# Optimization experiments

Hardware: AMD Instinct MI355X
Metric: run time of the kernel (lower is better)

## Reference

```python
import jax, jax.numpy as jnp
import numpy as np

H, KV, D, HID = 32, 8, 128, 4096
B, S = 1, 2048
ROPE_THETA = 10000.0


def setup_inputs() -> dict:
    key = jax.random.key(0)
    ks = jax.random.split(key, 5)
    std = 0.02
    return {
        "x": jax.random.normal(ks[0], (B, S, HID), jnp.float32),
        "Wq": jax.random.normal(ks[1], (H * D, HID), jnp.float32) * std,
        "Wk": jax.random.normal(ks[2], (KV * D, HID), jnp.float32) * std,
        "Wv": jax.random.normal(ks[3], (KV * D, HID), jnp.float32) * std,
        "Wo": jax.random.normal(ks[4], (HID, H * D), jnp.float32) * std,
    }


def _rope_cos_sin(seq_len, dim, dtype):
    inv_freq = 1.0 / (ROPE_THETA ** (jnp.arange(0, dim, 2, dtype=jnp.float32) / dim))
    t = jnp.arange(seq_len, dtype=jnp.float32)
    freqs = jnp.einsum("s,d->sd", t, inv_freq)          # [S, D/2]
    emb = jnp.concatenate([freqs, freqs], axis=-1)        # [S, D]
    return jnp.cos(emb).astype(dtype), jnp.sin(emb).astype(dtype)


def _rotate_half(x):
    x1, x2 = jnp.split(x, 2, axis=-1)
    return jnp.concatenate([-x2, x1], axis=-1)


def reference(x, Wq, Wk, Wv, Wo):
    Bx, Sx, _ = x.shape
    q = (x @ Wq.T).reshape(Bx, Sx, H, D).transpose(0, 2, 1, 3)    # [B,H,S,D]
    k = (x @ Wk.T).reshape(Bx, Sx, KV, D).transpose(0, 2, 1, 3)   # [B,KV,S,D]
    v = (x @ Wv.T).reshape(Bx, Sx, KV, D).transpose(0, 2, 1, 3)

    cos, sin = _rope_cos_sin(Sx, D, x.dtype)                       # [S,D]
    q = q * cos + _rotate_half(q) * sin
    k = k * cos + _rotate_half(k) * sin

    rep = H // KV
    k = jnp.repeat(k, rep, axis=1)                                 # [B,H,S,D]
    v = jnp.repeat(v, rep, axis=1)

    scale = 1.0 / jnp.sqrt(jnp.asarray(D, x.dtype))
    scores = jnp.einsum("bhqd,bhkd->bhqk", q, k) * scale           # [B,H,S,S]
    causal = jnp.tril(jnp.ones((Sx, Sx), dtype=bool))
    scores = jnp.where(causal, scores, jnp.asarray(-1e30, x.dtype))
    attn = jax.nn.softmax(scores, axis=-1)
    out = jnp.einsum("bhqk,bhkd->bhqd", attn, v)                   # [B,H,S,D]
    out = out.transpose(0, 2, 1, 3).reshape(Bx, Sx, H * D)
    return out @ Wo.T
```

## Files before the change

### kernel.cpp

```cpp
#include <hip/hip_runtime.h>

typedef unsigned short u16;
typedef unsigned int u32;

using f32x4  = __attribute__((ext_vector_type(4))) float;
using f32x16 = __attribute__((ext_vector_type(16))) float;
using bf16x8 = __attribute__((ext_vector_type(8))) __bf16;

#define S_LEN 2048
#define HID_DIM 4096
#define NH 32
#define NKV 8
#define HD 128
#define QKVN 6144

__device__ __forceinline__ u16 f2b(float f) {
  union { float f; u32 u; } v; v.f = f;
  u32 r = (v.u + 0x7FFFu + ((v.u >> 16) & 1u)) >> 16;
  return (u16)r;
}
__device__ __forceinline__ float b2f(u16 b) {
  union { u32 u; float f; } v; v.u = ((u32)b) << 16;
  return v.f;
}

__device__ __forceinline__ u32 cvtpk_bf16(float lo, float hi) {
  u32 r;
  asm("v_cvt_pk_bf16_f32 %0, %1, %2" : "=v"(r) : "v"(lo), "v"(hi));
  return r;
}
__device__ __forceinline__ void plane_swap(u32& a, u32& b) {
  asm volatile("v_permlane32_swap_b32 %0, %1" : "+v"(a), "+v"(b));
}

#define AS1 __attribute__((address_space(1)))
#define AS3 __attribute__((address_space(3)))
__device__ __forceinline__ void gl_lds16(const u16* g, u16* l) {
  __builtin_amdgcn_global_load_lds((const AS1 u32*)g, (AS3 u32*)l, 16, 0, 0);
}

#define SBAR  __builtin_amdgcn_s_barrier()
#define SCHED0 __builtin_amdgcn_sched_barrier(0)
#define LGKM0 do { asm volatile("s_waitcnt lgkmcnt(0)" ::: "memory"); SCHED0; } while (0)
#define PRIO1 __builtin_amdgcn_s_setprio(1)
#define PRIO0 __builtin_amdgcn_s_setprio(0)

template <int N> __device__ __forceinline__ void waitv() {
  if constexpr (N == 0)      asm volatile("s_waitcnt vmcnt(0)" ::: "memory");
  else if constexpr (N == 6) asm volatile("s_waitcnt vmcnt(6)" ::: "memory");
  else if constexpr (N == 7) asm volatile("s_waitcnt vmcnt(7)" ::: "memory");
  else                       asm volatile("s_waitcnt vmcnt(0)" ::: "memory");
  SCHED0;
}

__global__ void cast_kernel(const float* __restrict__ src, u16* __restrict__ dst, int n4) {
  int i = blockIdx.x * blockDim.x + threadIdx.x;
  int stride = gridDim.x * blockDim.x;
  for (; i < n4; i += stride) {
    float4 v = ((const float4*)src)[i];
    uint2 o;
    o.x = (u32)f2b(v.x) | ((u32)f2b(v.y) << 16);
    o.y = (u32)f2b(v.z) | ((u32)f2b(v.w) << 16);
    ((uint2*)dst)[i] = o;
  }
}


#define STAGE(DST, SRC, CH, LDK)                                   \
  _Pragma("unroll") for (int c = 0; c < (CH); ++c) {               \
    int d_ = c * 8192 + tid * 16;                                  \
    int rw_ = d_ >> 7;                                             \
    int cb_ = (d_ & 127) ^ ((rw_ & 7) << 4);                       \
    gl_lds16((SRC) + (size_t)rw_ * (LDK) + (cb_ >> 1), (DST) + (d_ >> 1)); \
  }

#define RDA(ABUF, MLO, KS)                                                    \
  _Pragma("unroll") for (int mm = 0; mm < 4; ++mm)                            \
    af[(MLO) + mm][KS] = *(const bf16x8*)((const char*)(ABUF) +               \
      (wmo + ((MLO) + mm) * 16 + lr) * 128 + (((((KS) << 2) | lg) ^ lr7) << 4));

#define RDB(BBUF, KS)                                                         \
  _Pragma("unroll") for (int nn = 0; nn < NF; ++nn)                           \
    bfr[nn][KS] = *(const bf16x8*)((const char*)(BBUF) +                      \
      (wno + nn * 16 + lr) * 128 + (((((KS) << 2) | lg) ^ lr7) << 4));

#define MFMA_Q(MLO, KS)                                                       \
  _Pragma("unroll") for (int mm = 0; mm < 4; ++mm)                            \
  _Pragma("unroll") for (int nn = 0; nn < NF; ++nn)                           \
    acc[(MLO) + mm][nn] = __builtin_amdgcn_mfma_f32_16x16x32_bf16(            \
        af[(MLO) + mm][KS], bfr[nn][KS], acc[(MLO) + mm][nn], 0, 0, 0);

template <int BN, int WN, int CBF>
__global__ __launch_bounds__(512, 2) void gemm8p(
    const u16* __restrict__ A, const u16* __restrict__ B, void* __restrict__ Cout,
    int M, int N, int K)
{
  constexpr int BM = 256;
  constexpr int NF = WN / 16;
  constexpr int LA = BM / 64;
  constexpr int LB = BN / 64;
  constexpr int LT = LA + LB;
  extern __shared__ __align__(16) u16 smem[];
  u16* const As0 = smem;
  u16* const Bs0 = smem + 2 * BM * 64;

  const int tid  = threadIdx.x;
  const int lane = tid & 63;
  const int wave = tid >> 6;
  const int lr  = lane & 15;
  const int lg  = lane >> 4;
  const int lr7 = lane & 7;

  const int nbx = N / BN;
  const int bid = blockIdx.x;
  const int cpx = gridDim.x >> 3;
  const int swz = (bid & 7) * cpx + (bid >> 3);
  const int bm = (swz / nbx) * BM;
  const int bn = (swz % nbx) * BN;
  const int wmo = (wave >> 2) * 128;
  const int wno = (wave & 3) * WN;

  const int NT = K >> 6;

  f32x4 acc[8][NF] = {};
  bf16x8 af[8][2], bfr[NF][2];

  const u16* aP = A + (size_t)bm * K;
  const u16* bP = B + (size_t)bn * K;

  STAGE(As0,           aP,      LA, K);
  STAGE(Bs0,           bP,      LB, K);
  STAGE(As0 + BM * 64, aP + 64, LA, K);
  STAGE(Bs0 + BN * 64, bP + 64, LB, K);
  waitv<LT>();
  SBAR; SCHED0;

  for (int t = 0; t < NT; ++t) {
    const int buf = t & 1;
    const u16* ab = As0 + buf * (BM * 64);
    const u16* bb = Bs0 + buf * (BN * 64);
    const bool st = (t + 2 < NT);

    RDA(ab, 0, 0); RDA(ab, 4, 0); RDB(bb, 0);
    LGKM0;
    PRIO1; MFMA_Q(0, 0); MFMA_Q(4, 0); PRIO0;
    RDA(ab, 0, 1); RDA(ab, 4, 1); RDB(bb, 1);
    LGKM0;
    SBAR;

    if (st) {
      STAGE(As0 + buf * (BM * 64), aP + (size_t)(t + 2) * 64, LA, K);
      STAGE(Bs0 + buf * (BN * 64), bP + (size_t)(t + 2) * 64, LB, K);
    }
    PRIO1; MFMA_Q(0, 1); MFMA_Q(4, 1); PRIO0;
    if (t + 1 < NT) {
      if (st) waitv<LT>(); else waitv<0>();
    }
    SBAR; SCHED0;
  }

#pragma unroll
  for (int m = 0; m < 8; ++m)
#pragma unroll
    for (int j = 0; j < 4; ++j) {
      int row = bm + wmo + m * 16 + lg * 4 + j;
      size_t base = (size_t)row * N + bn + wno + lr;
      if constexpr (CBF) {
        u16* C = (u16*)Cout;
#pragma unroll
        for (int nn = 0; nn < NF; ++nn) C[base + nn * 16] = f2b(acc[m][nn][j]);
      } else {
        float* C = (float*)Cout;
#pragma unroll
        for (int nn = 0; nn < NF; ++nn) C[base + nn * 16] = acc[m][nn][j];
      }
    }
}

__global__ void rope_qk(const u16* __restrict__ qkv, u16* __restrict__ dst,
                        int col_off, float scale, int frag) {
  int idx = blockIdx.x * blockDim.x + threadIdx.x;
  int i = idx & 63;
  int s = (idx >> 6) & (S_LEN - 1);
  int h = idx >> 17;
  const u16* row = qkv + (size_t)s * QKVN + col_off + h * HD;
  float a = b2f(row[i]);
  float b = b2f(row[i + 64]);
  float invf = __expf(-(float)i * 0.14391156831212787f);
  float f = (float)s * invf;
  float sn, cs;
  sincosf(f, &sn, &cs);
  float o1 = (a * cs - b * sn) * scale;
  float o2 = (b * cs + a * sn) * scale;
  if (frag) {
    int qt = h * 64 + (s >> 5);
    int qq = s & 31;
    int i2 = i + 64;
    dst[((qt * 8 + (i  >> 4)) * 2 + ((i  >> 3) & 1)) * 256 + qq * 8 + (i  & 7)] = f2b(o1);
    dst[((qt * 8 + (i2 >> 4)) * 2 + ((i2 >> 3) & 1)) * 256 + qq * 8 + (i2 & 7)] = f2b(o2);
  } else {
    u16* orow = dst + ((size_t)h * S_LEN + s) * HD;
    orow[i]      = f2b(o1);
    orow[i + 64] = f2b(o2);
  }
}

__global__ __launch_bounds__(256) void vf_pack(const u16* __restrict__ qkv,
                                               u16* __restrict__ VF) {
  __shared__ u16 vlds[32][136];
  const int bid = blockIdx.x;
  const int kv = bid >> 6, t = bid & 63;
  const int tid = threadIdx.x;
  const int r = tid >> 3, d0 = (tid & 7) * 16;
  const u16* src = qkv + (size_t)(t * 32 + r) * QKVN + 5120 + kv * HD + d0;
  *(bf16x8*)&vlds[r][d0]     = *(const bf16x8*)src;
  *(bf16x8*)&vlds[r][d0 + 8] = *(const bf16x8*)(src + 8);
  __syncthreads();
  u16* outt = VF + (size_t)bid * 4096;
#pragma unroll
  for (int g = 0; g < 2; ++g) {
    int G = tid + g * 256;
    int q = G & 31, dt = (G >> 5) & 3, hi2 = (G >> 7) & 1, kc = G >> 8;
    union { u16 u[8]; uint4 v; } o;
#pragma unroll
    for (int e = 0; e < 8; ++e)
      o.u[e] = vlds[kc * 16 + hi2 * 8 + e][dt * 32 + q];
    *(uint4*)&outt[G * 8] = o.v;
  }
}

__global__ __launch_bounds__(256, 2) void attn_fwd(
    const u16* __restrict__ QF,
    const u16* __restrict__ KF,
    const u16* __restrict__ VF,
    u16* __restrict__ Out)
{
  const int tid  = threadIdx.x;
  const int lane = tid & 63;
  const int wv   = tid >> 6;
  const int q31  = lane & 31;
  const int hi   = lane >> 5;
  const int bid  = blockIdx.x;
  const int kvh  = bid & 7;
  const int qi   = 63 - (bid >> 3);
  const int q0   = qi * 32;
  const int h    = kvh * 4 + wv;
  const int nt   = qi + 1;

  const u16* kbase = KF + (size_t)kvh * 64 * 4096 + hi * 256  + q31 * 8;
  const u16* vbase = VF + (size_t)kvh * 64 * 4096 + hi * 1024 + q31 * 8;

  bf16x8 qf[8];
  const u16* qfp = QF + (size_t)(h * 64 + qi) * 4096 + hi * 256 + q31 * 8;
#pragma unroll
  for (int dc = 0; dc < 8; ++dc)
    qf[dc] = *(const bf16x8*)(qfp + dc * 512);

  f32x16 o0 = {}, o1 = {}, o2 = {}, o3 = {};
  float m = -1e30f, lsum = 0.f;

  for (int t = 0; t < nt; ++t) {
    SBAR;

    bf16x8 kf[8];
    const u16* kfp = kbase + (size_t)t * 4096;
#pragma unroll
    for (int dc = 0; dc < 8; ++dc)
      kf[dc] = *(const bf16x8*)(kfp + dc * 512);

    bf16x8 vf[8];
    const u16* vfp = vbase + (size_t)t * 4096;
#pragma unroll
    for (int i = 0; i < 8; ++i)
      vf[i] = *(const bf16x8*)(vfp + (i & 1) * 2048 + (i >> 1) * 256);

    f32x16 st = {};
    PRIO1;
#pragma unroll
    for (int dc = 0; dc < 8; ++dc)
      st = __builtin_amdgcn_mfma_f32_32x32x16_bf16(kf[dc], qf[dc], st, 0, 0, 0);
    PRIO0;

    if (t == nt - 1) {
#pragma unroll
      for (int r = 0; r < 16; ++r) {
        int kk = (r & 3) + 8 * (r >> 2) + 4 * hi;
        if (kk > q31) st[r] = -1e30f;
      }
    }

    float a0 = fmaxf(st[0], st[1]),   a1 = fmaxf(st[2], st[3]);
    float a2 = fmaxf(st[4], st[5]),   a3 = fmaxf(st[6], st[7]);
    float a4 = fmaxf(st[8], st[9]),   a5 = fmaxf(st[10], st[11]);
    float a6 = fmaxf(st[12], st[13]), a7 = fmaxf(st[14], st[15]);
    a0 = fmaxf(a0, a1); a2 = fmaxf(a2, a3); a4 = fmaxf(a4, a5); a6 = fmaxf(a6, a7);
    float pmax = fmaxf(fmaxf(a0, a2), fmaxf(a4, a6));
    pmax = fmaxf(pmax, __shfl_xor(pmax, 32));

    if (__any(pmax > m + 8.f)) {
      float mn = fmaxf(m, pmax);
      float sf = exp2f(m - mn);
      m = mn;
      lsum *= sf;
#pragma unroll
      for (int r = 0; r < 16; ++r) { o0[r] *= sf; o1[r] *= sf; o2[r] *= sf; o3[r] *= sf; }
    }

    float ev[16];
#pragma unroll
    for (int r = 0; r < 16; ++r) ev[r] = exp2f(st[r] - m);
    float s0 = (ev[0] + ev[1]) + (ev[2] + ev[3]);
    float s1 = (ev[4] + ev[5]) + (ev[6] + ev[7]);
    float s2 = (ev[8] + ev[9]) + (ev[10] + ev[11]);
    float s3 = (ev[12] + ev[13]) + (ev[14] + ev[15]);
    float ps = (s0 + s1) + (s2 + s3);
    ps += __shfl_xor(ps, 32);
    lsum += ps;

    u32 c0 = cvtpk_bf16(ev[0],  ev[1]),  c1 = cvtpk_bf16(ev[2],  ev[3]);
    u32 c2 = cvtpk_bf16(ev[4],  ev[5]),  c3 = cvtpk_bf16(ev[6],  ev[7]);
    u32 c4 = cvtpk_bf16(ev[8],  ev[9]),  c5 = cvtpk_bf16(ev[10], ev[11]);
    u32 c6 = cvtpk_bf16(ev[12], ev[13]), c7 = cvtpk_bf16(ev[14], ev[15]);
    plane_swap(c0, c2);
    plane_swap(c1, c3);
    plane_swap(c4, c6);
    plane_swap(c5, c7);
    union { u32 u[4]; bf16x8 v; } pb0u, pb1u;
    pb0u.u[0] = c0; pb0u.u[1] = c1; pb0u.u[2] = c2; pb0u.u[3] = c3;
    pb1u.u[0] = c4; pb1u.u[1] = c5; pb1u.u[2] = c6; pb1u.u[3] = c7;

    PRIO1;
    o0 = __builtin_amdgcn_mfma_f32_32x32x16_bf16(vf[0], pb0u.v, o0, 0, 0, 0);
    o1 = __builtin_amdgcn_mfma_f32_32x32x16_bf16(vf[2], pb0u.v, o1, 0, 0, 0);
    o2 = __builtin_amdgcn_mfma_f32_32x32x16_bf16(vf[4], pb0u.v, o2, 0, 0, 0);
    o3 = __builtin_amdgcn_mfma_f32_32x32x16_bf16(vf[6], pb0u.v, o3, 0, 0, 0);
    o0 = __builtin_amdgcn_mfma_f32_32x32x16_bf16(vf[1], pb1u.v, o0, 0, 0, 0);
    o1 = __builtin_amdgcn_mfma_f32_32x32x16_bf16(vf[3], pb1u.v, o1, 0, 0, 0);
    o2 = __builtin_amdgcn_mfma_f32_32x32x16_bf16(vf[5], pb1u.v, o2, 0, 0, 0);
    o3 = __builtin_amdgcn_mfma_f32_32x32x16_bf16(vf[7], pb1u.v, o3, 0, 0, 0);
    PRIO0;
  }

  float inv = 1.0f / lsum;
  u16* orow = Out + (size_t)(q0 + q31) * (NH * HD) + h * HD;
#pragma unroll
  for (int dt = 0; dt < 4; ++dt) {
    const f32x16& oo = dt == 0 ? o0 : dt == 1 ? o1 : dt == 2 ? o2 : o3;
#pragma unroll
    for (int g = 0; g < 4; ++g) {
      ushort4 pk;
      pk.x = f2b(oo[g * 4 + 0] * inv);
      pk.y = f2b(oo[g * 4 + 1] * inv);
      pk.z = f2b(oo[g * 4 + 2] * inv);
      pk.w = f2b(oo[g * 4 + 3] * inv);
      *(ushort4*)&orow[dt * 32 + 8 * g + 4 * hi] = pk;
    }
  }
}

extern "C" void kernel_launch(void* const* d_in, const int* in_sizes, int n_in,
                              void* d_out, int out_size, void* d_ws, size_t ws_size,
                              hipStream_t stream) {
  const float* x  = (const float*)d_in[0];
  const float* Wq = (const float*)d_in[1];
  const float* Wk = (const float*)d_in[2];
  const float* Wv = (const float*)d_in[3];
  const float* Wo = (const float*)d_in[4];
  float* out = (float*)d_out;

  char* ws = (char*)d_ws;
  u16* xb   = (u16*)(ws);
  u16* wqkv = (u16*)(ws + (16ull << 20));
  u16* wo_b = (u16*)(ws + (64ull << 20));
  u16* qkvb = (u16*)(ws + (96ull << 20));
  u16* qb   = (u16*)(ws + (16ull << 20));
  u16* kfb  = (u16*)(ws + (32ull << 20));
  u16* vfb  = (u16*)(ws + (36ull << 20));
  u16* ao   = (u16*)(ws);

  const int smem_q = (256 + 192) * 256;
  const int smem_o = (256 + 128) * 256;
  hipFuncSetAttribute((const void*)&gemm8p<192, 48, 1>,
                      hipFuncAttributeMaxDynamicSharedMemorySize, smem_q);
  hipFuncSetAttribute((const void*)&gemm8p<128, 32, 0>,
                      hipFuncAttributeMaxDynamicSharedMemorySize, smem_o);

  cast_kernel<<<4096, 256, 0, stream>>>(x,  xb,   (2048 * 4096) / 4);
  cast_kernel<<<4096, 256, 0, stream>>>(Wq, wqkv, (4096 * 4096) / 4);
  cast_kernel<<<2048, 256, 0, stream>>>(Wk, wqkv + (size_t)4096 * 4096, (1024 * 4096) / 4);
  cast_kernel<<<2048, 256, 0, stream>>>(Wv, wqkv + (size_t)5120 * 4096, (1024 * 4096) / 4);
  cast_kernel<<<4096, 256, 0, stream>>>(Wo, wo_b, (4096 * 4096) / 4);

  gemm8p<192, 48, 1><<<256, 512, smem_q, stream>>>(xb, wqkv, qkvb, 2048, 6144, 4096);

  rope_qk<<<(32 * 2048 * 64) / 256, 256, 0, stream>>>(qkvb, qb,  0,    0.12751741f, 1);
  rope_qk<<<(8  * 2048 * 64) / 256, 256, 0, stream>>>(qkvb, kfb, 4096, 1.0f,        1);
  vf_pack<<<512, 256, 0, stream>>>(qkvb, vfb);

  attn_fwd<<<512, 256, 0, stream>>>(qb, kfb, vfb, ao);

  gemm8p<128, 32, 0><<<256, 512, smem_o, stream>>>(ao, wo_b, out, 2048, 4096, 4096);
}
```

Baseline: 312.9 us.

## Add finer-grained pipelined QKV GEMM and retile output projection GEMM

Adds a new QKV projection GEMM kernel that splits each K-step into four M-quarter MFMA phases. Global-to-LDS staging of the next tile is interleaved across those phases with a shallower vmcnt wait, to overlap loads with compute more finely and cut the live A-fragment registers. The output projection GEMM is generalized over BM and switched to a 128x256 tile with 64-wide wave columns, which changes reuse and the register footprint. The extra barriers per step add sync overhead and risk stalls.

```diff
diff --git a/kernel.cpp b/kernel.cpp
--- a/kernel.cpp
+++ b/kernel.cpp
@@ -47,6 +47,7 @@
 
 template <int N> __device__ __forceinline__ void waitv() {
   if constexpr (N == 0)      asm volatile("s_waitcnt vmcnt(0)" ::: "memory");
+  else if constexpr (N == 3) asm volatile("s_waitcnt vmcnt(3)" ::: "memory");
   else if constexpr (N == 6) asm volatile("s_waitcnt vmcnt(6)" ::: "memory");
   else if constexpr (N == 7) asm volatile("s_waitcnt vmcnt(7)" ::: "memory");
   else                       asm volatile("s_waitcnt vmcnt(0)" ::: "memory");
@@ -65,7 +66,6 @@
   }
 }
 
-
 #define STAGE(DST, SRC, CH, LDK)                                   \
   _Pragma("unroll") for (int c = 0; c < (CH); ++c) {               \
     int d_ = c * 8192 + tid * 16;                                  \
@@ -74,6 +74,109 @@
     gl_lds16((SRC) + (size_t)rw_ * (LDK) + (cb_ >> 1), (DST) + (d_ >> 1)); \
   }
 
+#define RAF(S, MQ)                                                            \
+  _Pragma("unroll") for (int j = 0; j < 2; ++j)                               \
+  _Pragma("unroll") for (int ks = 0; ks < 2; ++ks)                            \
+    af[j][ks] = *(const bf16x8*)((const char*)(As + (S)*16384) +              \
+      (wmo + (MQ)*32 + j*16 + lr) * 128 + ((((ks << 2) | lg) ^ lr7) << 4));
+
+#define RBF(S)                                                                \
+  _Pragma("unroll") for (int nn = 0; nn < 3; ++nn)                            \
+  _Pragma("unroll") for (int ks = 0; ks < 2; ++ks)                            \
+    bfr[nn][ks] = *(const bf16x8*)((const char*)(Bs + (S)*12288) +            \
+      (wno + nn*16 + lr) * 128 + ((((ks << 2) | lg) ^ lr7) << 4));
+
+#define MQUAD(MQ)                                                             \
+  _Pragma("unroll") for (int ks = 0; ks < 2; ++ks)                            \
+  _Pragma("unroll") for (int j = 0; j < 2; ++j)                               \
+  _Pragma("unroll") for (int nn = 0; nn < 3; ++nn)                            \
+    acc[(MQ)*2 + j][nn] = __builtin_amdgcn_mfma_f32_16x16x32_bf16(            \
+        af[j][ks], bfr[nn][ks], acc[(MQ)*2 + j][nn], 0, 0, 0);
+
+#define SGA(T, H) if ((T) < NT) { STAGE(As + ((T)&1)*16384 + (H)*8192,        \
+      aP + (size_t)((H)*128) * K + (size_t)(T)*64, 2, K); }
+#define SGB(T)    if ((T) < NT) { STAGE(Bs + ((T)&1)*12288,                   \
+      bP + (size_t)(T)*64, 3, K); }
+
+__global__ __launch_bounds__(512, 2) void gemm8s(
+    const u16* __restrict__ A, const u16* __restrict__ B, u16* __restrict__ C,
+    int M, int N, int K)
+{
+  extern __shared__ __align__(16) u16 smem[];
+  u16* const As = smem;
+  u16* const Bs = smem + 32768;
+
+  const int tid  = threadIdx.x;
+  const int lane = tid & 63;
+  const int wave = tid >> 6;
+  const int lr  = lane & 15;
+  const int lg  = lane >> 4;
+  const int lr7 = lane & 7;
+
+  const int nbx = N / 192;
+  const int bid = blockIdx.x;
+  const int cpx = gridDim.x >> 3;
+  const int swz = (bid & 7) * cpx + (bid >> 3);
+  const int bm = (swz / nbx) * 256;
+  const int bn = (swz % nbx) * 192;
+  const int wmo = (wave >> 2) * 128;
+  const int wno = (wave & 3) * 48;
+
+  const int NT = K >> 6;
+
+  f32x4 acc[8][3] = {};
+  bf16x8 af[2][2], bfr[3][2];
+
+  const u16* aP = A + (size_t)bm * K;
+  const u16* bP = B + (size_t)bn * K;
+
+  SGA(0, 0); SGA(0, 1); SGB(0); SGB(1);
+  waitv<3>();
+  SBAR; SCHED0;
+
+  for (int E = 0; E < NT; E += 2) {
+    const int O = E + 1;
+    RAF(0, 0); RBF(0); SGA(O, 0);
+    SCHED0; SBAR; LGKM0;
+    PRIO1; MQUAD(0); PRIO0; SBAR; SCHED0;
+    RAF(0, 1); SGA(O, 1); SGB(E + 2);
+    SCHED0; SBAR; LGKM0;
+    PRIO1; MQUAD(1); PRIO0; SBAR; SCHED0;
+    RAF(0, 2);
+    SCHED0; SBAR; LGKM0;
+    PRIO1; MQUAD(2); PRIO0; SBAR; SCHED0;
+    RAF(0, 3);
+    SCHED0; SBAR; LGKM0;
+    PRIO1; MQUAD(3); PRIO0;
+    if (E + 2 < NT) waitv<3>(); else waitv<0>();
+    SBAR; SCHED0;
+    RAF(1, 0); RBF(1); SGA(E + 2, 0);
+    SCHED0; SBAR; LGKM0;
+    PRIO1; MQUAD(0); PRIO0; SBAR; SCHED0;
+    RAF(1, 1); SGA(E + 2, 1); SGB(O + 2);
+    SCHED0; SBAR; LGKM0;
+    PRIO1; MQUAD(1); PRIO0; SBAR; SCHED0;
+    RAF(1, 2);
+    SCHED0; SBAR; LGKM0;
+    PRIO1; MQUAD(2); PRIO0; SBAR; SCHED0;
+    RAF(1, 3);
+    SCHED0; SBAR; LGKM0;
+    PRIO1; MQUAD(3); PRIO0;
+    if (O + 2 < NT) waitv<3>(); else waitv<0>();
+    SBAR; SCHED0;
+  }
+
+#pragma unroll
+  for (int m = 0; m < 8; ++m)
+#pragma unroll
+    for (int j = 0; j < 4; ++j) {
+      int row = bm + wmo + m * 16 + lg * 4 + j;
+      size_t base = (size_t)row * N + bn + wno + lr;
+#pragma unroll
+      for (int nn = 0; nn < 3; ++nn) C[base + nn * 16] = f2b(acc[m][nn][j]);
+    }
+}
+
 #define RDA(ABUF, MLO, KS)                                                    \
   _Pragma("unroll") for (int mm = 0; mm < 4; ++mm)                            \
     af[(MLO) + mm][KS] = *(const bf16x8*)((const char*)(ABUF) +               \
@@ -90,12 +193,12 @@
     acc[(MLO) + mm][nn] = __builtin_amdgcn_mfma_f32_16x16x32_bf16(            \
         af[(MLO) + mm][KS], bfr[nn][KS], acc[(MLO) + mm][nn], 0, 0, 0);
 
-template <int BN, int WN, int CBF>
+template <int BM, int BN, int WN, int CBF>
 __global__ __launch_bounds__(512, 2) void gemm8p(
     const u16* __restrict__ A, const u16* __restrict__ B, void* __restrict__ Cout,
     int M, int N, int K)
 {
-  constexpr int BM = 256;
+  constexpr int MF = BM / 32;
   constexpr int NF = WN / 16;
   constexpr int LA = BM / 64;
   constexpr int LB = BN / 64;
@@ -117,13 +220,13 @@
   const int swz = (bid & 7) * cpx + (bid >> 3);
   const int bm = (swz / nbx) * BM;
   const int bn = (swz % nbx) * BN;
-  const int wmo = (wave >> 2) * 128;
+  const int wmo = (wave >> 2) * (BM / 2);
   const int wno = (wave & 3) * WN;
 
   const int NT = K >> 6;
 
-  f32x4 acc[8][NF] = {};
-  bf16x8 af[8][2], bfr[NF][2];
+  f32x4 acc[MF][NF] = {};
+  bf16x8 af[MF][2], bfr[NF][2];
 
   const u16* aP = A + (size_t)bm * K;
   const u16* bP = B + (size_t)bn * K;
@@ -141,10 +244,14 @@
     const u16* bb = Bs0 + buf * (BN * 64);
     const bool st = (t + 2 < NT);
 
-    RDA(ab, 0, 0); RDA(ab, 4, 0); RDB(bb, 0);
+    RDA(ab, 0, 0);
+    if constexpr (MF == 8) { RDA(ab, 4, 0); }
+    RDB(bb, 0);
     LGKM0;
-    PRIO1; MFMA_Q(0, 0); MFMA_Q(4, 0); PRIO0;
-    RDA(ab, 0, 1); RDA(ab, 4, 1); RDB(bb, 1);
+    PRIO1; MFMA_Q(0, 0); if constexpr (MF == 8) { MFMA_Q(4, 0); } PRIO0;
+    RDA(ab, 0, 1);
+    if constexpr (MF == 8) { RDA(ab, 4, 1); }
+    RDB(bb, 1);
     LGKM0;
     SBAR;
 
@@ -152,7 +259,7 @@
       STAGE(As0 + buf * (BM * 64), aP + (size_t)(t + 2) * 64, LA, K);
       STAGE(Bs0 + buf * (BN * 64), bP + (size_t)(t + 2) * 64, LB, K);
     }
-    PRIO1; MFMA_Q(0, 1); MFMA_Q(4, 1); PRIO0;
+    PRIO1; MFMA_Q(0, 1); if constexpr (MF == 8) { MFMA_Q(4, 1); } PRIO0;
     if (t + 1 < NT) {
       if (st) waitv<LT>(); else waitv<0>();
     }
@@ -160,7 +267,7 @@
   }
 
 #pragma unroll
-  for (int m = 0; m < 8; ++m)
+  for (int m = 0; m < MF; ++m)
 #pragma unroll
     for (int j = 0; j < 4; ++j) {
       int row = bm + wmo + m * 16 + lg * 4 + j;
@@ -378,11 +485,11 @@
   u16* vfb  = (u16*)(ws + (36ull << 20));
   u16* ao   = (u16*)(ws);
 
-  const int smem_q = (256 + 192) * 256;
-  const int smem_o = (256 + 128) * 256;
-  hipFuncSetAttribute((const void*)&gemm8p<192, 48, 1>,
-                      hipFuncAttributeMaxDynamicSharedMemorySize, smem_q);
-  hipFuncSetAttribute((const void*)&gemm8p<128, 32, 0>,
+  const int smem_s = (2 * 16384 + 2 * 12288) * 2;
+  const int smem_o = (128 + 256) * 64 * 2 * 2;
+  hipFuncSetAttribute((const void*)&gemm8s,
+                      hipFuncAttributeMaxDynamicSharedMemorySize, smem_s);
+  hipFuncSetAttribute((const void*)&gemm8p<128, 256, 64, 0>,
                       hipFuncAttributeMaxDynamicSharedMemorySize, smem_o);
 
   cast_kernel<<<4096, 256, 0, stream>>>(x,  xb,   (2048 * 4096) / 4);
@@ -391,7 +498,7 @@
   cast_kernel<<<2048, 256, 0, stream>>>(Wv, wqkv + (size_t)5120 * 4096, (1024 * 4096) / 4);
   cast_kernel<<<4096, 256, 0, stream>>>(Wo, wo_b, (4096 * 4096) / 4);
 
-  gemm8p<192, 48, 1><<<256, 512, smem_q, stream>>>(xb, wqkv, qkvb, 2048, 6144, 4096);
+  gemm8s<<<256, 512, smem_s, stream>>>(xb, wqkv, qkvb, 2048, 6144, 4096);
 
   rope_qk<<<(32 * 2048 * 64) / 256, 256, 0, stream>>>(qkvb, qb,  0,    0.12751741f, 1);
   rope_qk<<<(8  * 2048 * 64) / 256, 256, 0, stream>>>(qkvb, kfb, 4096, 1.0f,        1);
@@ -399,5 +506,5 @@
 
   attn_fwd<<<512, 256, 0, stream>>>(qb, kfb, vfb, ao);
 
-  gemm8p<128, 32, 0><<<256, 512, smem_o, stream>>>(ao, wo_b, out, 2048, 4096, 4096);
-}
+  gemm8p<128, 256, 64, 0><<<256, 512, smem_o, stream>>>(ao, wo_b, out, 2048, 4096, 4096);
+}
```

Result: no change. 315.0 us (+0.7%).
